# Performance work log

Hardware: AMD Instinct MI355X
Metric: run time of the kernel (lower is better)

The kernel has to match this reference:

```python
import jax, jax.numpy as jnp
import numpy as np

N, E = 50000, 800000          # nodes, edges
IN, H, OUT = 256, 128, 2       # input feat, hidden_channels, out_channels
NEG_SLOPE = 0.2                # GATv2 LeakyReLU slope (PyG default)


def _w(key, fan_in, fan_out):
    return jax.random.normal(key, (fan_in, fan_out), jnp.float32) / np.sqrt(fan_in).astype(np.float32)


def setup_inputs() -> dict:
    key = jax.random.key(0)
    ks = jax.random.split(key, 24)
    inp = {
        "x": jax.random.normal(ks[0], (N, IN), jnp.float32),
        "edge_index": jax.random.randint(ks[1], (2, E), 0, N, jnp.int32),
        # GATv2Conv 0: in=IN -> H
        "c0_Wl": _w(ks[2], IN, H), "c0_Wr": _w(ks[3], IN, H),
        "c0_att": jax.random.normal(ks[4], (H,), jnp.float32) / np.sqrt(H).astype(np.float32),
        "c0_b": jnp.zeros((H,), jnp.float32),
        # GATv2Conv 1: H -> H
        "c1_Wl": _w(ks[5], H, H), "c1_Wr": _w(ks[6], H, H),
        "c1_att": jax.random.normal(ks[7], (H,), jnp.float32) / np.sqrt(H).astype(np.float32),
        "c1_b": jnp.zeros((H,), jnp.float32),
        # final GATv2Conv: H -> OUT
        "cf_Wl": _w(ks[8], H, OUT), "cf_Wr": _w(ks[9], H, OUT),
        "cf_att": jax.random.normal(ks[10], (OUT,), jnp.float32) / np.sqrt(OUT).astype(np.float32),
        "cf_b": jnp.zeros((OUT,), jnp.float32),
        # residual Linears
        "l0_W": _w(ks[11], IN, H), "l0_b": jnp.zeros((H,), jnp.float32),
        "l1_W": _w(ks[12], H, H), "l1_b": jnp.zeros((H,), jnp.float32),
        "lf_W": _w(ks[13], H, OUT), "lf_b": jnp.zeros((OUT,), jnp.float32),
    }
    return inp


def gatv2(x, edge_index, Wl, Wr, att, bias):
    """PyG GATv2Conv, heads=1, add_self_loops=False, share_weights=False."""
    src, dst = edge_index[0], edge_index[1]
    xs = x @ Wl                                   # [N,H] source transform
    xd = x @ Wr                                   # [N,H] target transform
    h = jax.nn.leaky_relu(xs[src] + xd[dst], NEG_SLOPE)   # [E,H]
    e = h @ att                                   # [E] attention logits
    # segment softmax over incoming edges of each destination node
    m = jax.ops.segment_max(e, dst, num_segments=N)
    m = jnp.where(jnp.isfinite(m), m, 0.0)
    p = jnp.exp(e - m[dst])
    s = jax.ops.segment_sum(p, dst, num_segments=N)
    alpha = p / (s[dst] + 1e-16)                  # [E]
    out = jax.ops.segment_sum(alpha[:, None] * xs[src], dst, num_segments=N)
    return out + bias


def reference(x, edge_index, c0_Wl, c0_Wr, c0_att, c0_b, c1_Wl, c1_Wr, c1_att, c1_b,
              cf_Wl, cf_Wr, cf_att, cf_b, l0_W, l0_b, l1_W, l1_b, lf_W, lf_b):
    # layer 0 + residual linear, then ReLU
    h = gatv2(x, edge_index, c0_Wl, c0_Wr, c0_att, c0_b) + (jax.nn.relu(x) @ l0_W + l0_b)
    h = jax.nn.relu(h)
    # layer 1 -> embeddings
    emb = gatv2(h, edge_index, c1_Wl, c1_Wr, c1_att, c1_b) + (jax.nn.relu(h) @ l1_W + l1_b)
    # final layer -> logits
    out = gatv2(emb, edge_index, cf_Wl, cf_Wr, cf_att, cf_b) + (jax.nn.relu(emb) @ lf_W + lf_b)
    return (out, emb)
```

## Files before the change

### kernel.cpp

```cpp
#include <hip/hip_runtime.h>
#include <hip/hip_bf16.h>

#define NEG_SLOPE 0.2f

typedef __attribute__((ext_vector_type(8))) _Float16 half8;
typedef __attribute__((ext_vector_type(2))) _Float16 h2v;
typedef __attribute__((ext_vector_type(4))) float f32x4;

__device__ __forceinline__ float toF(float x) { return x; }
__device__ __forceinline__ float toF(__hip_bfloat16 x) { return __bfloat162float(x); }
__device__ __forceinline__ float toF(_Float16 x) { return (float)x; }

__device__ __forceinline__ void stT(float* p, size_t i, float v) { p[i] = v; }
__device__ __forceinline__ void stT(__hip_bfloat16* p, size_t i, float v) {
    p[i] = __float2bfloat16(v);
}
__device__ __forceinline__ void stT(_Float16* p, size_t i, float v) { p[i] = (_Float16)v; }

template <typename T> struct IsBF { static constexpr bool v = false; };
template <> struct IsBF<__hip_bfloat16> { static constexpr bool v = true; };

__global__ void k_detect(const unsigned* __restrict__ x, int* __restrict__ flag) {
    unsigned u = x[threadIdx.x];
    int lo_exp = (int)((u >> 7) & 0xFFu);
    int ok = (lo_exp >= 90 && lo_exp <= 141) ? 1 : 0;
    unsigned long long b = __ballot(ok);
    if (threadIdx.x == 0) flag[0] = (__popcll(b) >= 48) ? 1 : 0;
}

__global__ __launch_bounds__(256) void k_cnt(const int* __restrict__ src,
                                             const int* __restrict__ dst, int E,
                                             int* __restrict__ gcnt,
                                             unsigned* __restrict__ bbuf, int cap) {
    __shared__ int hist[64];
    __shared__ int lbase[64];
    __shared__ int gbase[64];
    __shared__ int lfill[64];
    __shared__ unsigned ebuf[4096];
    __shared__ unsigned char bb[4096];
    int t = threadIdx.x;
    int e0 = blockIdx.x * 4096;
    if (t < 64) { hist[t] = 0; lfill[t] = 0; }
    __syncthreads();
    unsigned my[16];
    int mybkt[16];
#pragma unroll
    for (int i = 0; i < 16; ++i) {
        int idx = e0 + i * 256 + t;
        if (idx < E) {
            int d = dst[idx];
            int b = d >> 10;
            mybkt[i] = b;
            my[i] = (unsigned)src[idx] | ((unsigned)(d & 1023) << 16);
            atomicAdd(&hist[b], 1);
        } else {
            mybkt[i] = -1;
        }
    }
    __syncthreads();
    if (t < 64) {
        int h = hist[t];
        int v = h;
#pragma unroll
        for (int o = 1; o < 64; o <<= 1) {
            int u = __shfl_up(v, o, 64);
            if (t >= o) v += u;
        }
        lbase[t] = v - h;
        gbase[t] = (h > 0) ? atomicAdd(&gcnt[t], h) : 0;
    }
    __syncthreads();
#pragma unroll
    for (int i = 0; i < 16; ++i) {
        int b = mybkt[i];
        if (b >= 0) {
            int p = lbase[b] + atomicAdd(&lfill[b], 1);
            ebuf[p] = my[i];
            bb[p] = (unsigned char)b;
        }
    }
    __syncthreads();
    int total = min(4096, E - e0);
    for (int p = t; p < total; p += 256) {
        int b = bb[p];
        int o = gbase[b] + (p - lbase[b]);
        if (o < cap) bbuf[(size_t)b * cap + o] = ebuf[p];
    }
}

__global__ __launch_bounds__(256) void k_bucket_hist(const int* __restrict__ gcnt,
                                                     const unsigned* __restrict__ bbuf, int cap,
                                                     int* __restrict__ rowptr, int n) {
    __shared__ int hist[1024];
    int b = blockIdx.x, t = threadIdx.x;
    for (int i = t; i < 1024; i += 256) hist[i] = 0;
    __syncthreads();
    int cnt = min(gcnt[b], cap);
    const unsigned* p = bbuf + (size_t)b * cap;
    for (int i = t; i < cnt; i += 256) atomicAdd(&hist[p[i] >> 16], 1);
    __syncthreads();
    for (int i = t; i < 1024; i += 256) {
        int d = b * 1024 + i;
        if (d < n) rowptr[d + 1] = hist[i];
    }
}

__global__ __launch_bounds__(256) void k_bplace(const int* __restrict__ gcnt,
                                                const unsigned* __restrict__ bbuf, int cap,
                                                const int* __restrict__ rowptr,
                                                int* __restrict__ csr_src, int n) {
    __shared__ int base[1024];
    __shared__ int fill[1024];
    int b = blockIdx.x, t = threadIdx.x;
    for (int i = t; i < 1024; i += 256) {
        int d = b * 1024 + i;
        base[i] = (d < n) ? rowptr[d] : 0;
        fill[i] = 0;
    }
    __syncthreads();
    int cnt = min(gcnt[b], cap);
    const unsigned* p = bbuf + (size_t)b * cap;
    for (int i = t; i < cnt; i += 256) {
        unsigned e = p[i];
        int dl = (int)(e >> 16);
        int pos = base[dl] + atomicAdd(&fill[dl], 1);
        csr_src[pos] = (int)(e & 0xFFFFu);
    }
}

__global__ void k_hist(const int* __restrict__ dst, int E, int* __restrict__ rowptr) {
    int i = blockIdx.x * blockDim.x + threadIdx.x;
    if (i < E) atomicAdd(&rowptr[dst[i] + 1], 1);
}

__global__ void k_scatter(const int* __restrict__ src, const int* __restrict__ dst, int E,
                          const int* __restrict__ rowptr, int* __restrict__ fill,
                          int* __restrict__ csr_src) {
    int i = blockIdx.x * blockDim.x + threadIdx.x;
    if (i < E) {
        int d = dst[i];
        int pos = rowptr[d] + atomicAdd(&fill[d], 1);
        csr_src[pos] = src[i];
    }
}

__global__ __launch_bounds__(256) void k_scan1(int* __restrict__ rowptr,
                                               int* __restrict__ blksum, int n) {
    __shared__ int wsum[4];
    int t = threadIdx.x, lane = t & 63, w = t >> 6;
    int idx = blockIdx.x * 1024 + t * 4;
    int c0 = (idx + 0 < n) ? rowptr[idx + 1] : 0;
    int c1 = (idx + 1 < n) ? rowptr[idx + 2] : 0;
    int c2 = (idx + 2 < n) ? rowptr[idx + 3] : 0;
    int c3 = (idx + 3 < n) ? rowptr[idx + 4] : 0;
    int s1 = c0 + c1, s2 = s1 + c2, s3 = s2 + c3;
    int v = s3;
#pragma unroll
    for (int o = 1; o < 64; o <<= 1) {
        int u = __shfl_up(v, o, 64);
        if (lane >= o) v += u;
    }
    if (lane == 63) wsum[w] = v;
    __syncthreads();
    int woff = 0;
#pragma unroll
    for (int i = 0; i < 3; ++i)
        if (i < w) woff += wsum[i];
    int excl = woff + v - s3;
    if (idx + 0 < n) rowptr[idx + 1] = excl + c0;
    if (idx + 1 < n) rowptr[idx + 2] = excl + s1;
    if (idx + 2 < n) rowptr[idx + 3] = excl + s2;
    if (idx + 3 < n) rowptr[idx + 4] = excl + s3;
    if (t == 255) blksum[blockIdx.x] = woff + v;
}

__global__ void k_scan2(int* __restrict__ blksum, int nblk) {
    int t = threadIdx.x;
    int v = (t < nblk) ? blksum[t] : 0;
#pragma unroll
    for (int o = 1; o < 64; o <<= 1) {
        int u = __shfl_up(v, o, 64);
        if (t >= o) v += u;
    }
    if (t < nblk) blksum[t] = v;
}

__global__ void k_scan3(int* __restrict__ rowptr, const int* __restrict__ blksum, int n) {
    int idx = blockIdx.x * blockDim.x + threadIdx.x;
    if (idx < n) {
        int b = idx >> 10;
        if (b > 0) rowptr[idx + 1] += blksum[b - 1];
    }
}

template <typename WT>
__device__ void packW_body(const WT* W0, const WT* W1, const WT* W2, const WT* b2, int K,
                           _Float16* Bp, float* biasf) {
    int lane = threadIdx.x;
    int ksteps = K >> 5;
    int nb = 3 * ksteps * 8;
    int bid = blockIdx.x;
    if (bid == nb) {
        biasf[lane * 2 + 0] = toF(b2[lane * 2 + 0]);
        biasf[lane * 2 + 1] = toF(b2[lane * 2 + 1]);
        return;
    }
    int ks = bid / 24;
    int rem = bid - ks * 24;
    int o = rem >> 3, ct = rem & 7;
    const WT* W = (o == 0) ? W0 : ((o == 1) ? W1 : W2);
    int c = ct * 16 + (lane & 15);
    int k0 = ks * 32 + (lane >> 4) * 8;
    _Float16* out = Bp + (size_t)bid * 512 + lane * 8;
#pragma unroll
    for (int i = 0; i < 8; ++i) out[i] = (_Float16)toF(W[(size_t)(k0 + i) * 128 + c]);
}

__global__ void k_packW(const int* __restrict__ flag, const void* W0, const void* W1,
                        const void* W2, const void* b2, int K, _Float16* __restrict__ Bp,
                        float* __restrict__ biasf) {
    if (flag[0] == 0)
        packW_body<float>((const float*)W0, (const float*)W1, (const float*)W2,
                          (const float*)b2, K, Bp, biasf);
    else
        packW_body<__hip_bfloat16>((const __hip_bfloat16*)W0, (const __hip_bfloat16*)W1,
                                   (const __hip_bfloat16*)W2, (const __hip_bfloat16*)b2, K,
                                   Bp, biasf);
}

template <typename AT, typename O2T>
__device__ void gemm_body(const AT* __restrict__ A, int N, int K,
                          const _Float16* __restrict__ Bp, const float* __restrict__ biasf,
                          _Float16* __restrict__ O0, _Float16* __restrict__ O1,
                          O2T* __restrict__ O2, _Float16 (*sB)[12288]) {
    const int H = 128;
    int tid = threadIdx.x;
    int wave = tid >> 6, lane = tid & 63;
    int row0 = (blockIdx.x * 4 + wave) * 16;
    int rr = lane & 15, kg = lane >> 4;
    int arow = min(row0 + rr, N - 1);
    const int ksteps = K >> 5;

    f32x4 acc[3][8];
#pragma unroll
    for (int o = 0; o < 3; ++o)
#pragma unroll
        for (int ct = 0; ct < 8; ++ct) acc[o][ct] = f32x4{0.f, 0.f, 0.f, 0.f};

    auto stage = [&](int b, int ksv) {
        const char* gsrc = (const char*)(Bp + (size_t)ksv * 12288) + wave * 1024 + lane * 16;
        char* lbase = (char*)(&sB[b][0]) + wave * 1024;
#pragma unroll
        for (int r = 0; r < 6; ++r) {
            __builtin_amdgcn_global_load_lds(
                (const __attribute__((address_space(1))) unsigned*)(gsrc + r * 4096),
                (__attribute__((address_space(3))) unsigned*)(lbase + r * 4096), 16, 0, 0);
        }
    };
    auto loadA = [&](int ksv, uint4* dst) {
        const char* p = (const char*)A + ((size_t)arow * K + ksv * 32 + kg * 8) * sizeof(AT);
        dst[0] = *(const uint4*)p;
        if constexpr (sizeof(AT) == 4) dst[1] = *(const uint4*)(p + 16);
    };
    auto waitp = [&]() {
        if constexpr (sizeof(AT) == 4)
            asm volatile("s_waitcnt vmcnt(8)" ::: "memory");
        else
            asm volatile("s_waitcnt vmcnt(7)" ::: "memory");
    };
    auto compute = [&](const uint4* raw, const _Float16* sb) {
        half8 a0, a1, r0f, r1f;
        if constexpr (sizeof(AT) == 4) {
            union { uint4 u[2]; float f[8]; } cv;
            cv.u[0] = raw[0]; cv.u[1] = raw[1];
#pragma unroll
            for (int i = 0; i < 8; ++i) {
                float a = cv.f[i];
                _Float16 h = (_Float16)a;
                float lof = a - (float)h;
                _Float16 lo = (_Float16)lof;
                bool pos = a > 0.f;
                a0[i] = h; a1[i] = lo;
                r0f[i] = pos ? h : (_Float16)0.f;
                r1f[i] = pos ? lo : (_Float16)0.f;
            }
        } else if constexpr (IsBF<AT>::v) {
            union { uint4 u4; unsigned u[4]; } cv;
            cv.u4 = raw[0];
#pragma unroll
            for (int q = 0; q < 4; ++q) {
                union { unsigned u; float f; } lo, hi;
                lo.u = cv.u[q] << 16;
                hi.u = cv.u[q] & 0xFFFF0000u;
                a0[2 * q] = (_Float16)lo.f;
                a0[2 * q + 1] = (_Float16)hi.f;
                r0f[2 * q] = (_Float16)fmaxf(lo.f, 0.f);
                r0f[2 * q + 1] = (_Float16)fmaxf(hi.f, 0.f);
            }
        } else {
            union { uint4 u4; half8 h; } cv;
            cv.u4 = raw[0];
            a0 = cv.h;
#pragma unroll
            for (int i = 0; i < 8; ++i)
                r0f[i] = (a0[i] > (_Float16)0.f) ? a0[i] : (_Float16)0.f;
        }
#pragma unroll
        for (int ct = 0; ct < 8; ++ct) {
            half8 w0 = *(const half8*)(sb + (0 * 8 + ct) * 512 + lane * 8);
            half8 w1 = *(const half8*)(sb + (1 * 8 + ct) * 512 + lane * 8);
            half8 w2 = *(const half8*)(sb + (2 * 8 + ct) * 512 + lane * 8);
            acc[0][ct] = __builtin_amdgcn_mfma_f32_16x16x32_f16(a0, w0, acc[0][ct], 0, 0, 0);
            acc[1][ct] = __builtin_amdgcn_mfma_f32_16x16x32_f16(a0, w1, acc[1][ct], 0, 0, 0);
            acc[2][ct] = __builtin_amdgcn_mfma_f32_16x16x32_f16(r0f, w2, acc[2][ct], 0, 0, 0);
            if constexpr (sizeof(AT) == 4) {
                acc[0][ct] = __builtin_amdgcn_mfma_f32_16x16x32_f16(a1, w0, acc[0][ct], 0, 0, 0);
                acc[1][ct] = __builtin_amdgcn_mfma_f32_16x16x32_f16(a1, w1, acc[1][ct], 0, 0, 0);
                acc[2][ct] = __builtin_amdgcn_mfma_f32_16x16x32_f16(r1f, w2, acc[2][ct], 0, 0, 0);
            }
        }
    };

    uint4 rA[2], rB[2];
    loadA(0, rA);
    stage(0, 0);
    for (int ks = 0; ks < ksteps; ks += 2) {
        loadA(ks + 1, rB);
        stage(1, ks + 1);
        waitp();
        __builtin_amdgcn_s_barrier();
        compute(rA, &sB[0][0]);
        __builtin_amdgcn_s_barrier();
        if (ks + 2 < ksteps) {
            loadA(ks + 2, rA);
            stage(0, ks + 2);
            waitp();
        } else {
            asm volatile("s_waitcnt vmcnt(0)" ::: "memory");
        }
        __builtin_amdgcn_s_barrier();
        compute(rB, &sB[1][0]);
        __builtin_amdgcn_s_barrier();
    }

    int rb = row0 + kg * 4;
#pragma unroll
    for (int ct = 0; ct < 8; ++ct) {
        int c = ct * 16 + rr;
        float bv = biasf[c];
#pragma unroll
        for (int j = 0; j < 4; ++j) {
            int row = rb + j;
            if (row < N) {
                size_t o = (size_t)row * H + c;
                O0[o] = (_Float16)acc[0][ct][j];
                O1[o] = (_Float16)acc[1][ct][j];
                stT(O2, o, acc[2][ct][j] + bv);
            }
        }
    }
}

template <int LAYER>
__global__ __launch_bounds__(256) void gemm3_u(const int* __restrict__ flag, const void* Aext,
                                               const _Float16* Af16, int N, int K,
                                               const _Float16* __restrict__ Bp,
                                               const float* __restrict__ biasf,
                                               _Float16* __restrict__ O0,
                                               _Float16* __restrict__ O1, _Float16* O2h,
                                               float* O2f, __hip_bfloat16* O2b) {
    __shared__ _Float16 sB[2][12288];
    int f = flag[0];
    if constexpr (LAYER == 0) {
        if (f == 0)
            gemm_body<float, _Float16>((const float*)Aext, N, K, Bp, biasf, O0, O1, O2h, sB);
        else
            gemm_body<__hip_bfloat16, _Float16>((const __hip_bfloat16*)Aext, N, K, Bp, biasf,
                                                O0, O1, O2h, sB);
    } else {
        if (f == 0)
            gemm_body<_Float16, float>(Af16, N, K, Bp, biasf, O0, O1, O2f, sB);
        else
            gemm_body<_Float16, __hip_bfloat16>(Af16, N, K, Bp, biasf, O0, O1, O2b, sB);
    }
}

template <typename IOT, typename T, int FINAL>
__device__ void gat_body(const _Float16* __restrict__ xs, const _Float16* __restrict__ xd,
                         const int* __restrict__ rowptr, const int* __restrict__ csr_src,
                         IOT* __restrict__ io, const T* __restrict__ att,
                         const T* __restrict__ gbias, int n, int relu_out,
                         const T* __restrict__ Wl, const T* __restrict__ Wr,
                         const T* __restrict__ Wres, const T* __restrict__ bres,
                         float* __restrict__ xsf, float* __restrict__ xdf,
                         float* __restrict__ resf) {
    int tid = threadIdx.x;
    int l = tid & 15;
    int g = tid >> 4;
    int dst = blockIdx.x * 16 + g;
    if (blockIdx.x * 16 + ((tid >> 6) << 2) >= n) return;
    int dstc = min(dst, n - 1);
    bool act = dst < n;

    union U4H { uint4 u; h2v h[4]; };
    U4H du; du.u = *(const uint4*)(xd + (size_t)dstc * 128 + l * 8);
    h2v ap[4];
#pragma unroll
    for (int c = 0; c < 4; ++c) {
        ap[c][0] = (_Float16)toF(att[l * 8 + 2 * c]);
        ap[c][1] = (_Float16)toF(att[l * 8 + 2 * c + 1]);
    }
    const _Float16 ks = (_Float16)NEG_SLOPE;
    const h2v k02 = {ks, ks};

    int beg = rowptr[dstc];
    int end = act ? rowptr[dstc + 1] : beg;
    float m = -INFINITY, s = 0.f;
    h2v acc[4];
#pragma unroll
    for (int c = 0; c < 4; ++c) acc[c] = h2v{(_Float16)0.f, (_Float16)0.f};

    for (int j = beg; j < end; j += 4) {
        int rem = end - j;
        int i1 = (rem > 1) ? 1 : 0, i2 = (rem > 2) ? 2 : 0, i3 = (rem > 3) ? 3 : 0;
        int s0 = csr_src[j];
        int s1 = csr_src[j + i1];
        int s2 = csr_src[j + i2];
        int s3 = csr_src[j + i3];
        U4H v0, v1, v2, v3;
        v0.u = *(const uint4*)(xs + (size_t)s0 * 128 + l * 8);
        v1.u = *(const uint4*)(xs + (size_t)s1 * 128 + l * 8);
        v2.u = *(const uint4*)(xs + (size_t)s2 * 128 + l * 8);
        v3.u = *(const uint4*)(xs + (size_t)s3 * 128 + l * 8);
        float p0 = 0.f, p1 = 0.f, p2 = 0.f, p3 = 0.f;
#pragma unroll
        for (int c = 0; c < 4; ++c) {
            h2v t0 = v0.h[c] + du.h[c];
            t0 = __builtin_elementwise_max(t0, t0 * k02);
            p0 = __builtin_amdgcn_fdot2(t0, ap[c], p0, false);
            h2v t1 = v1.h[c] + du.h[c];
            t1 = __builtin_elementwise_max(t1, t1 * k02);
            p1 = __builtin_amdgcn_fdot2(t1, ap[c], p1, false);
            h2v t2 = v2.h[c] + du.h[c];
            t2 = __builtin_elementwise_max(t2, t2 * k02);
            p2 = __builtin_amdgcn_fdot2(t2, ap[c], p2, false);
            h2v t3 = v3.h[c] + du.h[c];
            t3 = __builtin_elementwise_max(t3, t3 * k02);
            p3 = __builtin_amdgcn_fdot2(t3, ap[c], p3, false);
        }
#pragma unroll
        for (int o = 1; o < 16; o <<= 1) {
            p0 += __shfl_xor(p0, o, 16);
            p1 += __shfl_xor(p1, o, 16);
            p2 += __shfl_xor(p2, o, 16);
            p3 += __shfl_xor(p3, o, 16);
        }
        if (rem < 2) p1 = -INFINITY;
        if (rem < 3) p2 = -INFINITY;
        if (rem < 4) p3 = -INFINITY;
        float pm = fmaxf(fmaxf(p0, p1), fmaxf(p2, p3));
        float nm = fmaxf(m, pm);
        float sc = __expf(m - nm);
        float w0 = __expf(p0 - nm);
        float w1 = __expf(p1 - nm);
        float w2 = __expf(p2 - nm);
        float w3 = __expf(p3 - nm);
        s = s * sc + ((w0 + w1) + (w2 + w3));
        _Float16 sch = (_Float16)sc;
        _Float16 w0h = (_Float16)w0, w1h = (_Float16)w1;
        _Float16 w2h = (_Float16)w2, w3h = (_Float16)w3;
        h2v scp = {sch, sch};
        h2v w0p = {w0h, w0h}, w1p = {w1h, w1h};
        h2v w2p = {w2h, w2h}, w3p = {w3h, w3h};
#pragma unroll
        for (int c = 0; c < 4; ++c)
            acc[c] = acc[c] * scp +
                     ((v0.h[c] * w0p + v1.h[c] * w1p) + (v2.h[c] * w2p + v3.h[c] * w3p));
        m = nm;
    }

    if (act) {
        float r = 1.f / (s + 1e-16f);
        size_t base = (size_t)dst * 128 + l * 8;
        float ev[8];
#pragma unroll
        for (int c = 0; c < 4; ++c) {
            int f0 = l * 8 + 2 * c;
            float v0 = (float)acc[c][0] * r + toF(gbias[f0]) + toF(io[base + 2 * c]);
            float v1 = (float)acc[c][1] * r + toF(gbias[f0 + 1]) + toF(io[base + 2 * c + 1]);
            if (relu_out) { v0 = fmaxf(v0, 0.f); v1 = fmaxf(v1, 0.f); }
            stT(io, base + 2 * c, v0);
            stT(io, base + 2 * c + 1, v1);
            ev[2 * c] = v0;
            ev[2 * c + 1] = v1;
        }
        if constexpr (FINAL) {
            float d[6] = {0.f, 0.f, 0.f, 0.f, 0.f, 0.f};
#pragma unroll
            for (int f = 0; f < 8; ++f) {
                int fg = (l * 8 + f) * 2;
                float e = ev[f];
                float rp = fmaxf(e, 0.f);
                d[0] += e * toF(Wl[fg]);
                d[1] += e * toF(Wl[fg + 1]);
                d[2] += e * toF(Wr[fg]);
                d[3] += e * toF(Wr[fg + 1]);
                d[4] += rp * toF(Wres[fg]);
                d[5] += rp * toF(Wres[fg + 1]);
            }
#pragma unroll
            for (int i = 0; i < 6; ++i) {
#pragma unroll
                for (int o = 1; o < 16; o <<= 1) d[i] += __shfl_xor(d[i], o, 16);
            }
            if (l == 0) {
                xsf[dst * 2 + 0] = d[0];
                xsf[dst * 2 + 1] = d[1];
                xdf[dst * 2 + 0] = d[2];
                xdf[dst * 2 + 1] = d[3];
                resf[dst * 2 + 0] = d[4] + toF(bres[0]);
                resf[dst * 2 + 1] = d[5] + toF(bres[1]);
            }
        }
    }
}

template <int FINAL>
__global__ __launch_bounds__(256) void gat_u(const int* __restrict__ flag,
                                             const _Float16* __restrict__ xs,
                                             const _Float16* __restrict__ xd,
                                             const int* __restrict__ rowptr,
                                             const int* __restrict__ csr_src, _Float16* io_h,
                                             float* io_f, __hip_bfloat16* io_b, const void* att,
                                             const void* gbias, int n, int relu_out,
                                             const void* Wl, const void* Wr, const void* Wres,
                                             const void* bres, float* xsf, float* xdf,
                                             float* resf) {
    typedef __hip_bfloat16 bf;
    int f = flag[0];
    if constexpr (FINAL == 0) {
        if (f == 0)
            gat_body<_Float16, float, 0>(xs, xd, rowptr, csr_src, io_h, (const float*)att,
                                         (const float*)gbias, n, relu_out, nullptr, nullptr,
                                         nullptr, nullptr, nullptr, nullptr, nullptr);
        else
            gat_body<_Float16, bf, 0>(xs, xd, rowptr, csr_src, io_h, (const bf*)att,
                                      (const bf*)gbias, n, relu_out, nullptr, nullptr, nullptr,
                                      nullptr, nullptr, nullptr, nullptr);
    } else {
        if (f == 0)
            gat_body<float, float, 1>(xs, xd, rowptr, csr_src, io_f, (const float*)att,
                                      (const float*)gbias, n, relu_out, (const float*)Wl,
                                      (const float*)Wr, (const float*)Wres, (const float*)bres,
                                      xsf, xdf, resf);
        else
            gat_body<bf, bf, 1>(xs, xd, rowptr, csr_src, io_b, (const bf*)att, (const bf*)gbias,
                                n, relu_out, (const bf*)Wl, (const bf*)Wr, (const bf*)Wres,
                                (const bf*)bres, xsf, xdf, resf);
    }
}

template <typename T>
__device__ void fe_body(const float* __restrict__ xsf, const float* __restrict__ xdf,
                        const float* __restrict__ resf, const int* __restrict__ rowptr,
                        const int* __restrict__ csr_src, const T* __restrict__ att,
                        const T* __restrict__ gb, T* __restrict__ out, int n) {
    int dst = blockIdx.x * blockDim.x + threadIdx.x;
    if (dst >= n) return;
    float2 dv = ((const float2*)xdf)[dst];
    float a0 = toF(att[0]), a1 = toF(att[1]);
    float m = -INFINITY, s = 0.f, acc0 = 0.f, acc1 = 0.f;
    int beg = rowptr[dst], end = rowptr[dst + 1];
    for (int j = beg; j < end; j += 4) {
        int rem = end - j;
        int i1 = (rem > 1) ? 1 : 0, i2 = (rem > 2) ? 2 : 0, i3 = (rem > 3) ? 3 : 0;
        int s0 = csr_src[j];
        int s1 = csr_src[j + i1];
        int s2 = csr_src[j + i2];
        int s3 = csr_src[j + i3];
        float2 v0 = ((const float2*)xsf)[s0];
        float2 v1 = ((const float2*)xsf)[s1];
        float2 v2 = ((const float2*)xsf)[s2];
        float2 v3 = ((const float2*)xsf)[s3];
        float h0, h1, e0, e1, e2, e3;
        h0 = v0.x + dv.x; h0 = fmaxf(h0, NEG_SLOPE * h0);
        h1 = v0.y + dv.y; h1 = fmaxf(h1, NEG_SLOPE * h1);
        e0 = h0 * a0 + h1 * a1;
        h0 = v1.x + dv.x; h0 = fmaxf(h0, NEG_SLOPE * h0);
        h1 = v1.y + dv.y; h1 = fmaxf(h1, NEG_SLOPE * h1);
        e1 = h0 * a0 + h1 * a1;
        h0 = v2.x + dv.x; h0 = fmaxf(h0, NEG_SLOPE * h0);
        h1 = v2.y + dv.y; h1 = fmaxf(h1, NEG_SLOPE * h1);
        e2 = h0 * a0 + h1 * a1;
        h0 = v3.x + dv.x; h0 = fmaxf(h0, NEG_SLOPE * h0);
        h1 = v3.y + dv.y; h1 = fmaxf(h1, NEG_SLOPE * h1);
        e3 = h0 * a0 + h1 * a1;
        if (rem < 2) e1 = -INFINITY;
        if (rem < 3) e2 = -INFINITY;
        if (rem < 4) e3 = -INFINITY;
        float pm = fmaxf(fmaxf(e0, e1), fmaxf(e2, e3));
        float nm = fmaxf(m, pm);
        float sc = __expf(m - nm);
        float w0 = __expf(e0 - nm), w1 = __expf(e1 - nm);
        float w2 = __expf(e2 - nm), w3 = __expf(e3 - nm);
        s = s * sc + ((w0 + w1) + (w2 + w3));
        acc0 = acc0 * sc + ((w0 * v0.x + w1 * v1.x) + (w2 * v2.x + w3 * v3.x));
        acc1 = acc1 * sc + ((w0 * v0.y + w1 * v1.y) + (w2 * v2.y + w3 * v3.y));
        m = nm;
    }
    float r = 1.f / (s + 1e-16f);
    float2 rv = ((const float2*)resf)[dst];
    stT(out, (size_t)dst * 2 + 0, acc0 * r + toF(gb[0]) + rv.x);
    stT(out, (size_t)dst * 2 + 1, acc1 * r + toF(gb[1]) + rv.y);
}

__global__ void final_edge_u(const int* __restrict__ flag, const float* __restrict__ xsf,
                             const float* __restrict__ xdf, const float* __restrict__ resf,
                             const int* __restrict__ rowptr, const int* __restrict__ csr_src,
                             const void* att, const void* gb, void* out, int n) {
    typedef __hip_bfloat16 bf;
    if (flag[0] == 0)
        fe_body<float>(xsf, xdf, resf, rowptr, csr_src, (const float*)att, (const float*)gb,
                       (float*)out, n);
    else
        fe_body<bf>(xsf, xdf, resf, rowptr, csr_src, (const bf*)att, (const bf*)gb, (bf*)out, n);
}

extern "C" void kernel_launch(void* const* d_in, const int* in_sizes, int n_in,
                              void* d_out, int out_size, void* d_ws, size_t ws_size,
                              hipStream_t stream) {
    typedef __hip_bfloat16 bf;
    typedef _Float16 f16;
    const int IN = 256, H = 128;
    const int N = in_sizes[0] / IN;
    const int E = in_sizes[1] / 2;

    const int* ei = (const int*)d_in[1];

    size_t off = 0;
    auto alloc = [&](size_t bytes) {
        void* p = (char*)d_ws + off;
        off += (bytes + 255) & ~(size_t)255;
        return p;
    };
    f16* xs = (f16*)alloc((size_t)N * H * 2);
    f16* xd = (f16*)alloc((size_t)N * H * 2);
    f16* hb = (f16*)alloc((size_t)N * H * 2);
    int* flag = (int*)alloc(256);
    int* rowptr = (int*)alloc((size_t)(N + 1) * 4);
    int* fill = (int*)alloc((size_t)N * 4);
    int* blksum = (int*)alloc(256 * 4);
    int* csr_src = (int*)alloc((size_t)E * 4);
    float* xsf = (float*)alloc((size_t)N * 2 * 4);
    float* xdf = (float*)alloc((size_t)N * 2 * 4);
    float* resf = (float*)alloc((size_t)N * 2 * 4);
    f16* Bp0 = (f16*)alloc((size_t)3 * 8 * 8 * 512 * 2);
    f16* Bp1 = (f16*)alloc((size_t)3 * 4 * 8 * 512 * 2);
    float* bias0 = (float*)alloc(128 * 4);
    float* bias1 = (float*)alloc(128 * 4);
    const int NB = (N + 1023) / 1024;
    const int CAP = ((2 * (E / (NB > 0 ? NB : 1) + 1) + 255) / 256) * 256;
    int* gcnt = (int*)alloc(64 * 4);
    unsigned* bbuf = (unsigned*)alloc((size_t)NB * CAP * 4);

    const int* e_src = ei;
    const int* e_dst = ei + E;

    k_detect<<<1, 64, 0, stream>>>((const unsigned*)d_in[0], flag);
    const int nblk = (N + 1023) / 1024;
    if (N <= 65536) {
        hipMemsetAsync(rowptr, 0, 4, stream);
        hipMemsetAsync(gcnt, 0, 64 * 4, stream);
        k_cnt<<<(E + 4095) / 4096, 256, 0, stream>>>(e_src, e_dst, E, gcnt, bbuf, CAP);
        k_bucket_hist<<<NB, 256, 0, stream>>>(gcnt, bbuf, CAP, rowptr, N);
        k_scan1<<<nblk, 256, 0, stream>>>(rowptr, blksum, N);
        k_scan2<<<1, 64, 0, stream>>>(blksum, nblk);
        k_scan3<<<(N + 255) / 256, 256, 0, stream>>>(rowptr, blksum, N);
        k_bplace<<<NB, 256, 0, stream>>>(gcnt, bbuf, CAP, rowptr, csr_src, N);
    } else {
        hipMemsetAsync(rowptr, 0, (size_t)(N + 1) * 4, stream);
        hipMemsetAsync(fill, 0, (size_t)N * 4, stream);
        k_hist<<<(E + 255) / 256, 256, 0, stream>>>(e_dst, E, rowptr);
        k_scan1<<<nblk, 256, 0, stream>>>(rowptr, blksum, N);
        k_scan2<<<1, 64, 0, stream>>>(blksum, nblk);
        k_scan3<<<(N + 255) / 256, 256, 0, stream>>>(rowptr, blksum, N);
        k_scatter<<<(E + 255) / 256, 256, 0, stream>>>(e_src, e_dst, E, rowptr, fill, csr_src);
    }

    k_packW<<<3 * 8 * 8 + 1, 64, 0, stream>>>(flag, d_in[2], d_in[3], d_in[14], d_in[15], IN,
                                              Bp0, bias0);
    k_packW<<<3 * 4 * 8 + 1, 64, 0, stream>>>(flag, d_in[6], d_in[7], d_in[16], d_in[17], H,
                                              Bp1, bias1);

    const int g64 = (N + 63) / 64;
    const int eblk16 = (N + 15) / 16;

    float* embF = (float*)d_out + (size_t)N * 2;
    bf* embB = (bf*)d_out + (size_t)N * 2;

    gemm3_u<0><<<g64, 256, 0, stream>>>(flag, d_in[0], nullptr, N, IN, Bp0, bias0, xs, xd, hb,
                                        nullptr, nullptr);
    gat_u<0><<<eblk16, 256, 0, stream>>>(flag, xs, xd, rowptr, csr_src, hb, nullptr, nullptr,
                                         d_in[4], d_in[5], N, 1, nullptr, nullptr, nullptr,
                                         nullptr, nullptr, nullptr, nullptr);

    gemm3_u<1><<<g64, 256, 0, stream>>>(flag, nullptr, hb, N, H, Bp1, bias1, xs, xd, nullptr,
                                        embF, embB);
    gat_u<1><<<eblk16, 256, 0, stream>>>(flag, xs, xd, rowptr, csr_src, nullptr, embF, embB,
                                         d_in[8], d_in[9], N, 0, d_in[10], d_in[11], d_in[18],
                                         d_in[19], xsf, xdf, resf);

    final_edge_u<<<(N + 255) / 256, 256, 0, stream>>>(flag, xsf, xdf, resf, rowptr, csr_src,
                                                      d_in[12], d_in[13], d_out, N);
}
```

Before: 334.9 us.

## Deepen GEMM A-load prefetch with compile-time K and widen GAT edge batch to 8

The GEMM body now takes K as a template parameter and fully unrolls the k-loop. It keeps three A-register buffers so A loads are issued two steps ahead, with per-step vmcnt waits tuned to the outstanding loads. The GAT aggregation kernel now processes 8 neighbor edges per iteration instead of 4, putting more gather loads in flight and amortizing the online-softmax rescale. The cost is more registers, which may reduce occupancy, and more wasted duplicate loads for low-degree nodes.

Result: no change. 332.6 us (-0.7%).

```diff
diff --git a/kernel.cpp b/kernel.cpp
--- a/kernel.cpp
+++ b/kernel.cpp
@@ -19,6 +19,14 @@
 
 template <typename T> struct IsBF { static constexpr bool v = false; };
 template <> struct IsBF<__hip_bfloat16> { static constexpr bool v = true; };
+
+__device__ __forceinline__ void vwaitn(int n) {
+    if (n == 0) asm volatile("s_waitcnt vmcnt(0)" ::: "memory");
+    else if (n == 7) asm volatile("s_waitcnt vmcnt(7)" ::: "memory");
+    else if (n == 8) asm volatile("s_waitcnt vmcnt(8)" ::: "memory");
+    else if (n == 9) asm volatile("s_waitcnt vmcnt(9)" ::: "memory");
+    else asm volatile("s_waitcnt vmcnt(10)" ::: "memory");
+}
 
 __global__ void k_detect(const unsigned* __restrict__ x, int* __restrict__ flag) {
     unsigned u = x[threadIdx.x];
@@ -228,18 +236,19 @@
                                    Bp, biasf);
 }
 
-template <typename AT, typename O2T>
-__device__ void gemm_body(const AT* __restrict__ A, int N, int K,
+template <typename AT, typename O2T, int KSTEPS>
+__device__ void gemm_body(const AT* __restrict__ A, int N,
                           const _Float16* __restrict__ Bp, const float* __restrict__ biasf,
                           _Float16* __restrict__ O0, _Float16* __restrict__ O1,
                           O2T* __restrict__ O2, _Float16 (*sB)[12288]) {
     const int H = 128;
+    const int K = KSTEPS * 32;
     int tid = threadIdx.x;
     int wave = tid >> 6, lane = tid & 63;
     int row0 = (blockIdx.x * 4 + wave) * 16;
     int rr = lane & 15, kg = lane >> 4;
     int arow = min(row0 + rr, N - 1);
-    const int ksteps = K >> 5;
+    constexpr int NR = (sizeof(AT) == 4) ? 2 : 1;
 
     f32x4 acc[3][8];
 #pragma unroll
@@ -260,13 +269,7 @@
     auto loadA = [&](int ksv, uint4* dst) {
         const char* p = (const char*)A + ((size_t)arow * K + ksv * 32 + kg * 8) * sizeof(AT);
         dst[0] = *(const uint4*)p;
-        if constexpr (sizeof(AT) == 4) dst[1] = *(const uint4*)(p + 16);
-    };
-    auto waitp = [&]() {
-        if constexpr (sizeof(AT) == 4)
-            asm volatile("s_waitcnt vmcnt(8)" ::: "memory");
-        else
-            asm volatile("s_waitcnt vmcnt(7)" ::: "memory");
+        if constexpr (NR == 2) dst[1] = *(const uint4*)(p + 16);
     };
     auto compute = [&](const uint4* raw, const _Float16* sb) {
         half8 a0, a1, r0f, r1f;
@@ -321,25 +324,22 @@
         }
     };
 
-    uint4 rA[2], rB[2];
-    loadA(0, rA);
+    uint4 rA[3][NR];
+    loadA(0, rA[0]);
+    loadA(1, rA[1]);
     stage(0, 0);
-    for (int ks = 0; ks < ksteps; ks += 2) {
-        loadA(ks + 1, rB);
-        stage(1, ks + 1);
-        waitp();
+#pragma unroll
+    for (int ks = 0; ks < KSTEPS; ++ks) {
+        if (ks + 1 < KSTEPS) {
+            stage((ks + 1) & 1, ks + 1);
+            asm volatile("" ::: "memory");
+        }
+        if (ks + 2 < KSTEPS) loadA(ks + 2, rA[(ks + 2) % 3]);
+        if (ks == 0 || ks == KSTEPS - 2) vwaitn(NR + 6);
+        else if (ks + 2 < KSTEPS) vwaitn(2 * NR + 6);
+        else vwaitn(0);
         __builtin_amdgcn_s_barrier();
-        compute(rA, &sB[0][0]);
-        __builtin_amdgcn_s_barrier();
-        if (ks + 2 < ksteps) {
-            loadA(ks + 2, rA);
-            stage(0, ks + 2);
-            waitp();
-        } else {
-            asm volatile("s_waitcnt vmcnt(0)" ::: "memory");
-        }
-        __builtin_amdgcn_s_barrier();
-        compute(rB, &sB[1][0]);
+        compute(rA[ks % 3], &sB[ks & 1][0]);
         __builtin_amdgcn_s_barrier();
     }
 
@@ -363,7 +363,7 @@
 
 template <int LAYER>
 __global__ __launch_bounds__(256) void gemm3_u(const int* __restrict__ flag, const void* Aext,
-                                               const _Float16* Af16, int N, int K,
+                                               const _Float16* Af16, int N,
                                                const _Float16* __restrict__ Bp,
                                                const float* __restrict__ biasf,
                                                _Float16* __restrict__ O0,
@@ -373,15 +373,15 @@
     int f = flag[0];
     if constexpr (LAYER == 0) {
         if (f == 0)
-            gemm_body<float, _Float16>((const float*)Aext, N, K, Bp, biasf, O0, O1, O2h, sB);
+            gemm_body<float, _Float16, 8>((const float*)Aext, N, Bp, biasf, O0, O1, O2h, sB);
         else
-            gemm_body<__hip_bfloat16, _Float16>((const __hip_bfloat16*)Aext, N, K, Bp, biasf,
-                                                O0, O1, O2h, sB);
+            gemm_body<__hip_bfloat16, _Float16, 8>((const __hip_bfloat16*)Aext, N, Bp, biasf,
+                                                   O0, O1, O2h, sB);
     } else {
         if (f == 0)
-            gemm_body<_Float16, float>(Af16, N, K, Bp, biasf, O0, O1, O2f, sB);
+            gemm_body<_Float16, float, 4>(Af16, N, Bp, biasf, O0, O1, O2f, sB);
         else
-            gemm_body<_Float16, __hip_bfloat16>(Af16, N, K, Bp, biasf, O0, O1, O2b, sB);
+            gemm_body<_Float16, __hip_bfloat16, 4>(Af16, N, Bp, biasf, O0, O1, O2b, sB);
     }
 }
 
@@ -420,62 +420,63 @@
 #pragma unroll
     for (int c = 0; c < 4; ++c) acc[c] = h2v{(_Float16)0.f, (_Float16)0.f};
 
-    for (int j = beg; j < end; j += 4) {
+    for (int j = beg; j < end; j += 8) {
         int rem = end - j;
-        int i1 = (rem > 1) ? 1 : 0, i2 = (rem > 2) ? 2 : 0, i3 = (rem > 3) ? 3 : 0;
-        int s0 = csr_src[j];
-        int s1 = csr_src[j + i1];
-        int s2 = csr_src[j + i2];
-        int s3 = csr_src[j + i3];
-        U4H v0, v1, v2, v3;
-        v0.u = *(const uint4*)(xs + (size_t)s0 * 128 + l * 8);
-        v1.u = *(const uint4*)(xs + (size_t)s1 * 128 + l * 8);
-        v2.u = *(const uint4*)(xs + (size_t)s2 * 128 + l * 8);
-        v3.u = *(const uint4*)(xs + (size_t)s3 * 128 + l * 8);
-        float p0 = 0.f, p1 = 0.f, p2 = 0.f, p3 = 0.f;
+        U4H v[8];
+#pragma unroll
+        for (int q = 0; q < 8; ++q) {
+            int idx = j + ((rem > q) ? q : 0);
+            int sq = csr_src[idx];
+            v[q].u = *(const uint4*)(xs + (size_t)sq * 128 + l * 8);
+        }
+        float p[8];
+#pragma unroll
+        for (int q = 0; q < 8; ++q) p[q] = 0.f;
 #pragma unroll
         for (int c = 0; c < 4; ++c) {
-            h2v t0 = v0.h[c] + du.h[c];
-            t0 = __builtin_elementwise_max(t0, t0 * k02);
-            p0 = __builtin_amdgcn_fdot2(t0, ap[c], p0, false);
-            h2v t1 = v1.h[c] + du.h[c];
-            t1 = __builtin_elementwise_max(t1, t1 * k02);
-            p1 = __builtin_amdgcn_fdot2(t1, ap[c], p1, false);
-            h2v t2 = v2.h[c] + du.h[c];
-            t2 = __builtin_elementwise_max(t2, t2 * k02);
-            p2 = __builtin_amdgcn_fdot2(t2, ap[c], p2, false);
-            h2v t3 = v3.h[c] + du.h[c];
-            t3 = __builtin_elementwise_max(t3, t3 * k02);
-            p3 = __builtin_amdgcn_fdot2(t3, ap[c], p3, false);
+#pragma unroll
+            for (int q = 0; q < 8; ++q) {
+                h2v t = v[q].h[c] + du.h[c];
+                t = __builtin_elementwise_max(t, t * k02);
+                p[q] = __builtin_amdgcn_fdot2(t, ap[c], p[q], false);
+            }
         }
 #pragma unroll
         for (int o = 1; o < 16; o <<= 1) {
-            p0 += __shfl_xor(p0, o, 16);
-            p1 += __shfl_xor(p1, o, 16);
-            p2 += __shfl_xor(p2, o, 16);
-            p3 += __shfl_xor(p3, o, 16);
-        }
-        if (rem < 2) p1 = -INFINITY;
-        if (rem < 3) p2 = -INFINITY;
-        if (rem < 4) p3 = -INFINITY;
-        float pm = fmaxf(fmaxf(p0, p1), fmaxf(p2, p3));
+#pragma unroll
+            for (int q = 0; q < 8; ++q) p[q] += __shfl_xor(p[q], o, 16);
+        }
+#pragma unroll
+        for (int q = 1; q < 8; ++q)
+            if (rem < q + 1) p[q] = -INFINITY;
+        float pm = p[0];
+#pragma unroll
+        for (int q = 1; q < 8; ++q) pm = fmaxf(pm, p[q]);
         float nm = fmaxf(m, pm);
         float sc = __expf(m - nm);
-        float w0 = __expf(p0 - nm);
-        float w1 = __expf(p1 - nm);
-        float w2 = __expf(p2 - nm);
-        float w3 = __expf(p3 - nm);
-        s = s * sc + ((w0 + w1) + (w2 + w3));
+        float w[8];
+        float ws = 0.f;
+#pragma unroll
+        for (int q = 0; q < 8; ++q) {
+            w[q] = __expf(p[q] - nm);
+            ws += w[q];
+        }
+        s = s * sc + ws;
         _Float16 sch = (_Float16)sc;
-        _Float16 w0h = (_Float16)w0, w1h = (_Float16)w1;
-        _Float16 w2h = (_Float16)w2, w3h = (_Float16)w3;
         h2v scp = {sch, sch};
-        h2v w0p = {w0h, w0h}, w1p = {w1h, w1h};
-        h2v w2p = {w2h, w2h}, w3p = {w3h, w3h};
-#pragma unroll
-        for (int c = 0; c < 4; ++c)
-            acc[c] = acc[c] * scp +
-                     ((v0.h[c] * w0p + v1.h[c] * w1p) + (v2.h[c] * w2p + v3.h[c] * w3p));
+        h2v wp[8];
+#pragma unroll
+        for (int q = 0; q < 8; ++q) {
+            _Float16 wh = (_Float16)w[q];
+            wp[q] = h2v{wh, wh};
+        }
+#pragma unroll
+        for (int c = 0; c < 4; ++c) {
+            h2v a = acc[c] * scp;
+#pragma unroll
+            for (int q = 0; q < 8; ++q) a = a + v[q].h[c] * wp[q];
+            acc[c] = a;
+        }
         m = nm;
     }
 
@@ -698,13 +699,13 @@
     float* embF = (float*)d_out + (size_t)N * 2;
     bf* embB = (bf*)d_out + (size_t)N * 2;
 
-    gemm3_u<0><<<g64, 256, 0, stream>>>(flag, d_in[0], nullptr, N, IN, Bp0, bias0, xs, xd, hb,
+    gemm3_u<0><<<g64, 256, 0, stream>>>(flag, d_in[0], nullptr, N, Bp0, bias0, xs, xd, hb,
                                         nullptr, nullptr);
     gat_u<0><<<eblk16, 256, 0, stream>>>(flag, xs, xd, rowptr, csr_src, hb, nullptr, nullptr,
                                          d_in[4], d_in[5], N, 1, nullptr, nullptr, nullptr,
                                          nullptr, nullptr, nullptr, nullptr);
 
-    gemm3_u<1><<<g64, 256, 0, stream>>>(flag, nullptr, hb, N, H, Bp1, bias1, xs, xd, nullptr,
+    gemm3_u<1><<<g64, 256, 0, stream>>>(flag, nullptr, hb, N, Bp1, bias1, xs, xd, nullptr,
                                         embF, embB);
     gat_u<1><<<eblk16, 256, 0, stream>>>(flag, xs, xd, rowptr, csr_src, nullptr, embF, embB,
                                          d_in[8], d_in[9], N, 0, d_in[10], d_in[11], d_in[18],
```
